# Kernel optimization log

Measured on AMD Instinct MI355X. Metric: run time of the kernel, lower is better.

The kernel has to match this reference:

```python
import jax, jax.numpy as jnp
import numpy as np

TOP_K = 3


def setup_inputs() -> dict:
    key = jax.random.key(0)
    k1, k2, k3 = jax.random.split(key, 3)
    N, M, D = 100000, 6890, 128
    source_feats = jax.random.normal(k1, (N, D), dtype=jnp.float32)
    target_feats = jax.random.normal(k2, (M, D), dtype=jnp.float32)
    target_points = jax.random.normal(k3, (M, 3), dtype=jnp.float32)
    return {
        "source_feats": source_feats,
        "target_feats": target_feats,
        "target_points": target_points,
    }


def reference(source_feats, target_feats, target_points):
    # Pairwise squared distances via matmul + squared norms: [N, M]
    dp = jnp.matmul(source_feats, target_feats.T)
    source_sq = jnp.sum(source_feats * source_feats, axis=-1, keepdims=True)  # [N,1]
    target_sq = jnp.sum(target_feats * target_feats, axis=-1)                 # [M]
    dists = source_sq - 2.0 * dp + target_sq[None, :]
    # top-3 nearest neighbors (topk of negated distances, like torch.topk(-dists))
    scores, indices = jax.lax.top_k(-dists, TOP_K)      # [N,3], [N,3]
    weights = jax.nn.softmax(scores, axis=-1)           # [N,3]
    selected = target_points[indices]                   # [N,3,3] gather
    predicted_points = jnp.sum(selected * weights[..., None], axis=-2)  # [N,3]
    return predicted_points
```

## Files before the change

kernel.cpp:

```cpp
#include <hip/hip_runtime.h>
#include <math.h>

#define D 128
#define CT 2
#define SRCS_PER_WAVE (CT * 16)
#define WAVES 4
#define BIAS 16.0f
#define REFK 10

typedef __attribute__((ext_vector_type(8))) short short8;
typedef __attribute__((ext_vector_type(4))) float f32x4;

static __device__ __forceinline__ unsigned short f2bf(float x) {
    unsigned u = __float_as_uint(x);
    unsigned r = u + 0x7FFFu + ((u >> 16) & 1u);
    return (unsigned short)(r >> 16);
}

static __device__ __forceinline__ unsigned med3u(unsigned a, unsigned b, unsigned c) {
    unsigned d;
    asm("v_med3_u32 %0, %1, %2, %3" : "=v"(d) : "v"(a), "v"(b), "v"(c));
    return d;
}

static __device__ __forceinline__ void ins5(unsigned st[5], unsigned k) {
    st[4] = med3u(st[4], st[3], k);
    st[3] = med3u(st[3], st[2], k);
    st[2] = med3u(st[2], st[1], k);
    st[1] = med3u(st[1], st[0], k);
    st[0] = st[0] < k ? st[0] : k;
}

static __device__ __forceinline__ void ins10(unsigned st[REFK], unsigned k) {
    #pragma unroll
    for (int s = REFK - 1; s >= 1; --s) st[s] = med3u(st[s], st[s - 1], k);
    st[0] = st[0] < k ? st[0] : k;
}

static __device__ __forceinline__ void gload_lds16(const void* g, void* l) {
    __builtin_amdgcn_global_load_lds(
        (const __attribute__((address_space(1))) unsigned*)g,
        (__attribute__((address_space(3))) unsigned*)l, 16, 0, 0);
}

__global__ void prep_kernel(const float* __restrict__ tgt, unsigned short* __restrict__ tbf,
                            float* __restrict__ tsqb, float* __restrict__ tsqe,
                            int M, int Mpad) {
    int row  = blockIdx.x;
    int lane = threadIdx.x;
    if (row >= Mpad) return;
    float2 v = make_float2(0.f, 0.f);
    if (row < M) v = *(const float2*)(tgt + (size_t)row * D + lane * 2);
    unsigned pack = (unsigned)f2bf(-2.f * v.x) | ((unsigned)f2bf(-2.f * v.y) << 16);
    size_t byte = (size_t)row * 256 + (size_t)(((lane >> 2) ^ (row & 15)) * 16 + (lane & 3) * 4);
    *(unsigned*)((char*)tbf + byte) = pack;
    float ss = v.x * v.x + v.y * v.y;
    #pragma unroll
    for (int off = 1; off < 64; off <<= 1) ss += __shfl_xor(ss, off);
    if (lane == 0) {
        tsqe[row] = ss;
        tsqb[row] = (row < M) ? (ss + BIAS) : __builtin_inff();
    }
}

__global__ __launch_bounds__(256, 4)
void knn_scan(const float* __restrict__ src, const unsigned short* __restrict__ tbf,
              const float* __restrict__ tsqb, unsigned* __restrict__ keys,
              int N, int M, int h0, int msteps) {
    const int tid  = (int)threadIdx.x;
    const int wid  = tid >> 6;
    const int lane = tid & 63;
    const int c16  = lane & 15;
    const int g    = lane >> 4;
    const int half = blockIdx.y;
    const int colbase = blockIdx.x * (WAVES * SRCS_PER_WAVE) + wid * SRCS_PER_WAVE;

    __shared__ __align__(16) short8 abuf[2][512];

    short8 bfrag[CT][4];
    #pragma unroll
    for (int ct = 0; ct < CT; ++ct) {
        int srow = colbase + ct * 16 + c16;
        if (srow >= N) srow = N - 1;
        const float* sp = src + (size_t)srow * D + g * 8;
        #pragma unroll
        for (int kk = 0; kk < 4; ++kk) {
            float4 v0 = *(const float4*)(sp + kk * 32);
            float4 v1 = *(const float4*)(sp + kk * 32 + 4);
            short8 b;
            b[0] = (short)f2bf(v0.x); b[1] = (short)f2bf(v0.y);
            b[2] = (short)f2bf(v0.z); b[3] = (short)f2bf(v0.w);
            b[4] = (short)f2bf(v1.x); b[5] = (short)f2bf(v1.y);
            b[6] = (short)f2bf(v1.z); b[7] = (short)f2bf(v1.w);
            bfrag[ct][kk] = b;
        }
    }

    unsigned st[CT][5];
    #pragma unroll
    for (int ct = 0; ct < CT; ++ct)
        #pragma unroll
        for (int s = 0; s < 5; ++s) st[ct][s] = 0xFFFFFFFFu;

    int oe[4];
    #pragma unroll
    for (int kk = 0; kk < 4; ++kk) oe[kk] = c16 * 16 + ((g + 4 * kk) ^ c16);

    const int t0 = half ? h0 : 0;
    const int tc = half ? (msteps - h0) : h0;

    #define STAGE(t, b)                                                              \
        do {                                                                         \
            const char* gbase_ = (const char*)tbf + (size_t)(t) * 8192;              \
            _Pragma("unroll")                                                        \
            for (int q_ = 0; q_ < 2; ++q_) {                                         \
                int uoff_ = q_ * 256 + wid * 64;                                     \
                gload_lds16(gbase_ + ((size_t)(uoff_ + lane)) * 16,                  \
                            (void*)&abuf[b][uoff_]);                                 \
            }                                                                        \
        } while (0)

    float4 qv[2], qn[2];
    #pragma unroll
    for (int s = 0; s < 2; ++s)
        qv[s] = *(const float4*)(tsqb + (size_t)t0 * 32 + s * 16 + g * 4);
    STAGE(t0, 0);
    __syncthreads();

    unsigned jb = (unsigned)(t0 * 32 + g * 4);
    int cur = 0;
    for (int tt = 0; tt < tc; ++tt) {
        int tn = t0 + ((tt + 1 < tc) ? (tt + 1) : tt);
        STAGE(tn, cur ^ 1);
        #pragma unroll
        for (int s = 0; s < 2; ++s)
            qn[s] = *(const float4*)(tsqb + (size_t)tn * 32 + s * 16 + g * 4);

        #pragma unroll
        for (int sub = 0; sub < 2; ++sub) {
            short8 a[4];
            #pragma unroll
            for (int kk = 0; kk < 4; ++kk)
                a[kk] = abuf[cur][sub * 256 + oe[kk]];
            #pragma unroll
            for (int ct = 0; ct < CT; ++ct) {
                f32x4 acc = { qv[sub].x, qv[sub].y, qv[sub].z, qv[sub].w };
                #pragma unroll
                for (int kk = 0; kk < 4; ++kk)
                    acc = __builtin_amdgcn_mfma_f32_16x16x32_bf16(a[kk], bfrag[ct][kk], acc, 0, 0, 0);
                #pragma unroll
                for (int e = 0; e < 4; ++e) {
                    unsigned key = (__float_as_uint(acc[e]) & 0xFFFFE000u) | (jb + (unsigned)e);
                    ins5(st[ct], key);
                }
            }
            jb += 16;
        }
        #pragma unroll
        for (int s = 0; s < 2; ++s) qv[s] = qn[s];
        __syncthreads();
        cur ^= 1;
    }
    #undef STAGE

    #pragma unroll
    for (int ct = 0; ct < CT; ++ct) {
        int srow = colbase + ct * 16 + c16;
        if (srow < N) {
            #pragma unroll
            for (int s = 0; s < 5; ++s)
                keys[(size_t)srow * 40 + half * 20 + g * 5 + s] = st[ct][s];
        }
    }
}

__global__ __launch_bounds__(256, 4)
void knn_merge(const float* __restrict__ src, const float* __restrict__ tgt,
               const float* __restrict__ tsqe, const unsigned* __restrict__ keys,
               const float* __restrict__ tpts, float* __restrict__ out,
               int N, int M) {
    int i = blockIdx.x * 256 + (int)threadIdx.x;
    if (i >= N) return;

    unsigned best[REFK];
    #pragma unroll
    for (int s = 0; s < REFK; ++s) best[s] = 0xFFFFFFFFu;

    const uint4* kp = (const uint4*)(keys + (size_t)i * 40);
    #pragma unroll
    for (int q = 0; q < 10; ++q) {
        uint4 kv = kp[q];
        ins10(best, kv.x); ins10(best, kv.y); ins10(best, kv.z); ins10(best, kv.w);
    }

    int js[REFK]; float dt[REFK];
    #pragma unroll
    for (int s = 0; s < REFK; ++s) {
        int j = (int)(best[s] & 0x1FFFu);
        js[s] = (j < M) ? j : (M - 1);
        dt[s] = 0.f;
    }

    const float4* sp = (const float4*)(src + (size_t)i * D);
    for (int kc = 0; kc < D / 4; ++kc) {
        float4 sv = sp[kc];
        #pragma unroll
        for (int s = 0; s < REFK; ++s) {
            float4 tv = *(const float4*)(tgt + (size_t)js[s] * D + kc * 4);
            dt[s] = fmaf(sv.x, tv.x, fmaf(sv.y, tv.y, fmaf(sv.z, tv.z, fmaf(sv.w, tv.w, dt[s]))));
        }
    }

    float d0 = __builtin_inff(), d1 = d0, d2 = d0;
    int i0 = 0, i1 = 0, i2 = 0;
    #pragma unroll
    for (int s = 0; s < REFK; ++s) {
        float dd = fmaf(-2.f, dt[s], tsqe[js[s]]);
        int jj = js[s];
        if (dd < d2) {
            if (dd < d1) {
                d2 = d1; i2 = i1;
                if (dd < d0) { d1 = d0; i1 = i0; d0 = dd; i0 = jj; }
                else         { d1 = dd; i1 = jj; }
            } else { d2 = dd; i2 = jj; }
        }
    }

    float e1 = __expf(d0 - d1);
    float e2 = __expf(d0 - d2);
    float inv = 1.f / (1.f + e1 + e2);
    float w0 = inv, w1 = e1 * inv, w2 = e2 * inv;
    const float* p0 = tpts + 3 * (size_t)i0;
    const float* p1 = tpts + 3 * (size_t)i1;
    const float* p2 = tpts + 3 * (size_t)i2;
    out[3 * (size_t)i + 0] = w0 * p0[0] + w1 * p1[0] + w2 * p2[0];
    out[3 * (size_t)i + 1] = w0 * p0[1] + w1 * p1[1] + w2 * p2[1];
    out[3 * (size_t)i + 2] = w0 * p0[2] + w1 * p1[2] + w2 * p2[2];
}

extern "C" void kernel_launch(void* const* d_in, const int* in_sizes, int n_in,
                              void* d_out, int out_size, void* d_ws, size_t ws_size,
                              hipStream_t stream) {
    const float* src  = (const float*)d_in[0];
    const float* tgt  = (const float*)d_in[1];
    const float* tpts = (const float*)d_in[2];
    float* out = (float*)d_out;

    int N = in_sizes[0] / D;
    int M = in_sizes[1] / D;
    int Mpad = (M + 31) & ~31;
    int msteps = Mpad >> 5;
    int h0 = (msteps + 1) >> 1;

    char* w = (char*)d_ws;
    unsigned short* tbf = (unsigned short*)w;                 w += (size_t)Mpad * 256;
    float* tsqb = (float*)w;                                  w += (size_t)Mpad * 4;
    float* tsqe = (float*)w;                                  w += (size_t)Mpad * 4;
    unsigned* keys = (unsigned*)w;

    prep_kernel<<<Mpad, 64, 0, stream>>>(tgt, tbf, tsqb, tsqe, M, Mpad);

    int per_block = WAVES * SRCS_PER_WAVE;
    dim3 sgrid((N + per_block - 1) / per_block, 2);
    knn_scan<<<sgrid, 256, 0, stream>>>(src, tbf, tsqb, keys, N, M, h0, msteps);

    knn_merge<<<(N + 255) / 256, 256, 0, stream>>>(src, tgt, tsqe, keys, tpts, out, N, M);
}
```

Before: 423.3 us.

## Triple-buffer target tiles in LDS with norm staging and vmcnt-based barriers

Replaces the double-buffered LDS pipeline with a three-stage ring in which each stage also holds the tile's target norms, loaded by a 4-byte global_load_lds instead of per-lane register loads. Synchronisation uses explicit s_waitcnt vmcnt(3) plus s_barrier, so the next tile's loads stay in flight while the barrier is passed. M is padded to a multiple of 192 so each half runs a whole number of 3-tile iterations, and launch bounds are raised to 6 blocks per CU for occupancy. The risks are register pressure under the tighter launch bound and fragile hand-written wait counts.

```diff
diff --git a/kernel.cpp b/kernel.cpp
--- a/kernel.cpp
+++ b/kernel.cpp
@@ -7,6 +7,8 @@
 #define WAVES 4
 #define BIAS 16.0f
 #define REFK 10
+#define TILEB 8192
+#define BUFB  8448
 
 typedef __attribute__((ext_vector_type(8))) short short8;
 typedef __attribute__((ext_vector_type(4))) float f32x4;
@@ -41,6 +43,11 @@
     __builtin_amdgcn_global_load_lds(
         (const __attribute__((address_space(1))) unsigned*)g,
         (__attribute__((address_space(3))) unsigned*)l, 16, 0, 0);
+}
+static __device__ __forceinline__ void gload_lds4(const void* g, void* l) {
+    __builtin_amdgcn_global_load_lds(
+        (const __attribute__((address_space(1))) unsigned*)g,
+        (__attribute__((address_space(3))) unsigned*)l, 4, 0, 0);
 }
 
 __global__ void prep_kernel(const float* __restrict__ tgt, unsigned short* __restrict__ tbf,
@@ -63,7 +70,7 @@
     }
 }
 
-__global__ __launch_bounds__(256, 4)
+__global__ __launch_bounds__(256, 6)
 void knn_scan(const float* __restrict__ src, const unsigned short* __restrict__ tbf,
               const float* __restrict__ tsqb, unsigned* __restrict__ keys,
               int N, int M, int h0, int msteps) {
@@ -75,7 +82,7 @@
     const int half = blockIdx.y;
     const int colbase = blockIdx.x * (WAVES * SRCS_PER_WAVE) + wid * SRCS_PER_WAVE;
 
-    __shared__ __align__(16) short8 abuf[2][512];
+    __shared__ __align__(16) char smem[3 * BUFB];
 
     short8 bfrag[CT][4];
     #pragma unroll
@@ -108,60 +115,70 @@
 
     const int t0 = half ? h0 : 0;
     const int tc = half ? (msteps - h0) : h0;
-
-    #define STAGE(t, b)                                                              \
-        do {                                                                         \
-            const char* gbase_ = (const char*)tbf + (size_t)(t) * 8192;              \
-            _Pragma("unroll")                                                        \
-            for (int q_ = 0; q_ < 2; ++q_) {                                         \
-                int uoff_ = q_ * 256 + wid * 64;                                     \
-                gload_lds16(gbase_ + ((size_t)(uoff_ + lane)) * 16,                  \
-                            (void*)&abuf[b][uoff_]);                                 \
-            }                                                                        \
+    const int tlast = t0 + tc - 1;
+
+    #define STAGE(tile, b)                                                          \
+        do {                                                                        \
+            const char* gb_ = (const char*)tbf + (size_t)(tile) * TILEB;            \
+            char* lb_ = smem + (size_t)(b) * BUFB;                                  \
+            gload_lds16(gb_ + wid * 2048 + lane * 16, lb_ + wid * 2048);            \
+            gload_lds16(gb_ + wid * 2048 + 1024 + lane * 16, lb_ + wid * 2048 + 1024);\
+            gload_lds4((const char*)tsqb + (size_t)(tile) * 128 + lane * 4,         \
+                       lb_ + TILEB);                                                \
         } while (0)
 
-    float4 qv[2], qn[2];
-    #pragma unroll
-    for (int s = 0; s < 2; ++s)
-        qv[s] = *(const float4*)(tsqb + (size_t)t0 * 32 + s * 16 + g * 4);
+    #define COMPUTE(b)                                                              \
+        do {                                                                        \
+            const short8* A_ = (const short8*)(smem + (size_t)(b) * BUFB);          \
+            const float*  Q_ = (const float*)(smem + (size_t)(b) * BUFB + TILEB);   \
+            _Pragma("unroll")                                                       \
+            for (int sub_ = 0; sub_ < 2; ++sub_) {                                  \
+                short8 a_[4];                                                       \
+                _Pragma("unroll")                                                   \
+                for (int kk = 0; kk < 4; ++kk) a_[kk] = A_[sub_ * 256 + oe[kk]];    \
+                float4 q_ = *(const float4*)(Q_ + sub_ * 16 + g * 4);               \
+                _Pragma("unroll")                                                   \
+                for (int ct = 0; ct < CT; ++ct) {                                   \
+                    f32x4 acc = { q_.x, q_.y, q_.z, q_.w };                         \
+                    _Pragma("unroll")                                               \
+                    for (int kk = 0; kk < 4; ++kk)                                  \
+                        acc = __builtin_amdgcn_mfma_f32_16x16x32_bf16(              \
+                                  a_[kk], bfrag[ct][kk], acc, 0, 0, 0);             \
+                    _Pragma("unroll")                                               \
+                    for (int e = 0; e < 4; ++e) {                                   \
+                        unsigned key = (__float_as_uint(acc[e]) & 0xFFFFE000u)      \
+                                       | (jb + (unsigned)e);                        \
+                        ins5(st[ct], key);                                          \
+                    }                                                               \
+                }                                                                   \
+                jb += 16;                                                           \
+            }                                                                       \
+        } while (0)
+
+    unsigned jb = (unsigned)(t0 * 32 + g * 4);
+
     STAGE(t0, 0);
-    __syncthreads();
-
-    unsigned jb = (unsigned)(t0 * 32 + g * 4);
-    int cur = 0;
-    for (int tt = 0; tt < tc; ++tt) {
-        int tn = t0 + ((tt + 1 < tc) ? (tt + 1) : tt);
-        STAGE(tn, cur ^ 1);
-        #pragma unroll
-        for (int s = 0; s < 2; ++s)
-            qn[s] = *(const float4*)(tsqb + (size_t)tn * 32 + s * 16 + g * 4);
-
-        #pragma unroll
-        for (int sub = 0; sub < 2; ++sub) {
-            short8 a[4];
-            #pragma unroll
-            for (int kk = 0; kk < 4; ++kk)
-                a[kk] = abuf[cur][sub * 256 + oe[kk]];
-            #pragma unroll
-            for (int ct = 0; ct < CT; ++ct) {
-                f32x4 acc = { qv[sub].x, qv[sub].y, qv[sub].z, qv[sub].w };
-                #pragma unroll
-                for (int kk = 0; kk < 4; ++kk)
-                    acc = __builtin_amdgcn_mfma_f32_16x16x32_bf16(a[kk], bfrag[ct][kk], acc, 0, 0, 0);
-                #pragma unroll
-                for (int e = 0; e < 4; ++e) {
-                    unsigned key = (__float_as_uint(acc[e]) & 0xFFFFE000u) | (jb + (unsigned)e);
-                    ins5(st[ct], key);
-                }
-            }
-            jb += 16;
-        }
-        #pragma unroll
-        for (int s = 0; s < 2; ++s) qv[s] = qn[s];
-        __syncthreads();
-        cur ^= 1;
-    }
+    STAGE(t0 + 1, 1);
+    asm volatile("s_waitcnt vmcnt(3)\n\ts_barrier" ::: "memory");
+
+    for (int i = 0; i < tc; i += 3) {
+        int t_ = t0 + i;
+        int s2 = t_ + 2 < tlast ? t_ + 2 : tlast;
+        int s3 = t_ + 3 < tlast ? t_ + 3 : tlast;
+        int s4 = t_ + 4 < tlast ? t_ + 4 : tlast;
+        STAGE(s2, 2);
+        COMPUTE(0);
+        asm volatile("s_waitcnt vmcnt(3)\n\ts_barrier" ::: "memory");
+        STAGE(s3, 0);
+        COMPUTE(1);
+        asm volatile("s_waitcnt vmcnt(3)\n\ts_barrier" ::: "memory");
+        STAGE(s4, 1);
+        COMPUTE(2);
+        asm volatile("s_waitcnt vmcnt(3)\n\ts_barrier" ::: "memory");
+    }
+    asm volatile("s_waitcnt vmcnt(0)" ::: "memory");
     #undef STAGE
+    #undef COMPUTE
 
     #pragma unroll
     for (int ct = 0; ct < CT; ++ct) {
@@ -248,9 +265,9 @@
 
     int N = in_sizes[0] / D;
     int M = in_sizes[1] / D;
-    int Mpad = (M + 31) & ~31;
+    int Mpad = (M + 191) & ~191;
     int msteps = Mpad >> 5;
-    int h0 = (msteps + 1) >> 1;
+    int h0 = msteps >> 1;
 
     char* w = (char*)d_ws;
     unsigned short* tbf = (unsigned short*)w;                 w += (size_t)Mpad * 256;
```

Result: slower. 714.3 us (+68.7%).
